# Kernel optimization log

Hardware: AMD Instinct MI355X
Metric: run time of the kernel (lower is better)

The kernel has to match this reference:

```python
import jax, jax.numpy as jnp
import numpy as np

D_K = 64  # per-head key dim, used for 1/sqrt(d_k) scaling


def setup_inputs() -> dict:
    key = jax.random.key(0)
    ks = jax.random.split(key, 9)
    B, S, D, H, DK, DV = 2, 4096, 512, 8, 64, 64
    s = 0.02
    return {
        "x": jax.random.normal(ks[0], (B, S, D), dtype=jnp.float32),
        "Wq": jax.random.normal(ks[1], (H, D, DK), dtype=jnp.float32) * s,
        "bq": jax.random.normal(ks[2], (H, DK), dtype=jnp.float32) * s,
        "Wk": jax.random.normal(ks[3], (H, D, DK), dtype=jnp.float32) * s,
        "bk": jax.random.normal(ks[4], (H, DK), dtype=jnp.float32) * s,
        "Wv": jax.random.normal(ks[5], (H, D, DV), dtype=jnp.float32) * s,
        "bv": jax.random.normal(ks[6], (H, DV), dtype=jnp.float32) * s,
        "Wo": jax.random.normal(ks[7], (H * DV, D), dtype=jnp.float32) * s,
        "bo": jax.random.normal(ks[8], (D,), dtype=jnp.float32) * s,
    }


def reference(x, Wq, bq, Wk, bk, Wv, bv, Wo, bo):
    # Per-head projections, vectorized over heads: [B,H,S,dk/dv]
    q = jnp.einsum("bsd,hdk->bhsk", x, Wq) + bq[None, :, None, :]
    k = jnp.einsum("bsd,hdk->bhsk", x, Wk) + bk[None, :, None, :]
    v = jnp.einsum("bsd,hdv->bhsv", x, Wv) + bv[None, :, None, :]
    # Scaled dot-product attention (no mask; dropout inactive at eval)
    scores = jnp.einsum("bhsk,bhtk->bhst", q, k) / jnp.sqrt(jnp.float32(D_K))
    attn = jax.nn.softmax(scores, axis=-1)
    o = jnp.einsum("bhst,bhtv->bhsv", attn, v)
    # Concat heads along feature dim: [B,S,H*dv]
    B, H, S, DV = o.shape
    concat = jnp.transpose(o, (0, 2, 1, 3)).reshape(B, S, H * DV)
    return concat @ Wo + bo
```

## Files before the change

kernel.cpp:

```cpp
#include <hip/hip_runtime.h>
#include <hip/hip_bf16.h>

typedef __attribute__((ext_vector_type(8))) short bf16x8;
typedef __attribute__((ext_vector_type(4))) float f32x4;
typedef __attribute__((ext_vector_type(16))) float f32x16;
typedef __attribute__((ext_vector_type(4))) unsigned short u16x4;
typedef __attribute__((ext_vector_type(4))) unsigned int u32x4;

#define NB 2
#define NS 4096
#define ND 512
#define NH 8

__device__ __forceinline__ unsigned short f2bf(float f) {
  unsigned int u = __float_as_uint(f);
  u += 0x7fffu + ((u >> 16) & 1u);
  return (unsigned short)(u >> 16);
}

__device__ __forceinline__ float bf2f(unsigned short h) {
  return __uint_as_float(((unsigned)h) << 16);
}

__device__ __forceinline__ float exp2_hw(float x) {
  float r;
  asm("v_exp_f32 %0, %1" : "=v"(r) : "v"(x));
  return r;
}

__device__ __forceinline__ unsigned cvtpk(float lo, float hi) {
  unsigned r;
  asm("v_cvt_pk_bf16_f32 %0, %1, %2" : "=v"(r) : "v"(lo), "v"(hi));
  return r;
}

__device__ __forceinline__ void swap32(unsigned& a, unsigned& b) {
  asm("v_permlane32_swap_b32 %0, %1" : "+v"(a), "+v"(b));
}

__device__ __forceinline__ bf16x8 mkfrag(unsigned w0, unsigned w1,
                                         unsigned w2, unsigned w3) {
  u32x4 u = {w0, w1, w2, w3};
  return __builtin_bit_cast(bf16x8, u);
}

__device__ __forceinline__ void gload_lds16(const unsigned short* g,
                                            unsigned short* l) {
  __builtin_amdgcn_global_load_lds(
      (const __attribute__((address_space(1))) unsigned int*)g,
      (__attribute__((address_space(3))) unsigned int*)l, 16, 0, 0);
}

__global__ void pack_kernel(const float* __restrict__ x,
                            const float* __restrict__ Wq,
                            const float* __restrict__ Wk,
                            const float* __restrict__ Wv,
                            const float* __restrict__ Wo,
                            unsigned short* __restrict__ x_bf,
                            unsigned short* __restrict__ w3,
                            unsigned short* __restrict__ wo_t)
{
  int idx = blockIdx.x * 256 + threadIdx.x;
  const int NX4 = NB * NS * ND / 4;
  const int NW = 512 * 512;
  if (idx < NX4) {
    const float4 f = ((const float4*)x)[idx];
    u16x4 o;
    o[0] = f2bf(f.x); o[1] = f2bf(f.y); o[2] = f2bf(f.z); o[3] = f2bf(f.w);
    ((u16x4*)x_bf)[idx] = o;
  } else if (idx < NX4 + 3 * NW) {
    int j = idx - NX4;
    int p = j / NW;
    int r = j - p * NW;
    int n = r >> 9, d = r & 511;
    int h = n >> 6, o = n & 63;
    const float* W = (p == 0) ? Wq : (p == 1) ? Wk : Wv;
    w3[j] = f2bf(W[(h * 512 + d) * 64 + o]);
  } else if (idx < NX4 + 4 * NW) {
    int j = idx - NX4 - 3 * NW;
    int n = j >> 9, kk = j & 511;
    wo_t[j] = f2bf(Wo[kk * 512 + n]);
  }
}

template <int MODE>
__global__ void gemm_bt(const unsigned short* __restrict__ A,
                        const unsigned short* __restrict__ Bm,
                        const float* __restrict__ b0,
                        const float* __restrict__ b1,
                        const float* __restrict__ b2,
                        unsigned short* __restrict__ qo,
                        unsigned short* __restrict__ ko,
                        unsigned short* __restrict__ vo,
                        float* __restrict__ fo) {
  __shared__ unsigned short Al[128 * 32];
  __shared__ unsigned short Bl[128 * 32];
  const int t = threadIdx.x;
  const int m0 = blockIdx.x * 128;
  const int n0 = blockIdx.y * 128;
  const int lane = t & 63;
  const int w = t >> 6;
  const int wm = w >> 1, wn = w & 1;
  const int c = lane & 15, g = lane >> 4;

  f32x4 acc[4][4];
#pragma unroll
  for (int i = 0; i < 4; ++i)
#pragma unroll
    for (int j = 0; j < 4; ++j) acc[i][j] = (f32x4){0.f, 0.f, 0.f, 0.f};

  const int srow = t >> 1, sseg = (t & 1) * 16;
  const unsigned short* Ap = A + (size_t)(m0 + srow) * 512 + sseg;
  const unsigned short* Bp = Bm + (size_t)(n0 + srow) * 512 + sseg;
  unsigned short* Alp = &Al[srow * 32 + sseg];
  unsigned short* Blp = &Bl[srow * 32 + sseg];

  for (int k0 = 0; k0 < 512; k0 += 32) {
    bf16x8 ra0 = *(const bf16x8*)(Ap + k0);
    bf16x8 ra1 = *(const bf16x8*)(Ap + k0 + 8);
    bf16x8 rb0 = *(const bf16x8*)(Bp + k0);
    bf16x8 rb1 = *(const bf16x8*)(Bp + k0 + 8);
    __syncthreads();
    *(bf16x8*)(Alp) = ra0;
    *(bf16x8*)(Alp + 8) = ra1;
    *(bf16x8*)(Blp) = rb0;
    *(bf16x8*)(Blp + 8) = rb1;
    __syncthreads();
    bf16x8 af[4], bfr[4];
#pragma unroll
    for (int mf = 0; mf < 4; ++mf)
      af[mf] = *(const bf16x8*)&Al[(wm * 64 + mf * 16 + c) * 32 + g * 8];
#pragma unroll
    for (int nf = 0; nf < 4; ++nf)
      bfr[nf] = *(const bf16x8*)&Bl[(wn * 64 + nf * 16 + c) * 32 + g * 8];
#pragma unroll
    for (int mf = 0; mf < 4; ++mf)
#pragma unroll
      for (int nf = 0; nf < 4; ++nf)
        acc[mf][nf] = __builtin_amdgcn_mfma_f32_16x16x32_bf16(
            af[mf], bfr[nf], acc[mf][nf], 0, 0, 0);
  }

  if (MODE == 0) {
    const int proj = n0 >> 9;
    const float* bias = proj == 0 ? b0 : (proj == 1 ? b1 : b2);
    unsigned short* dst01 = proj == 0 ? qo : ko;
    const float scale = proj == 0 ? 0.18033688011112042f : 1.0f;
#pragma unroll
    for (int nf = 0; nf < 4; ++nf) {
      const int col5 = (n0 + wn * 64 + nf * 16 + c) & 511;
      const int h = col5 >> 6, o = col5 & 63;
      const float bb = bias[col5];
#pragma unroll
      for (int mf = 0; mf < 4; ++mf) {
#pragma unroll
        for (int r = 0; r < 4; ++r) {
          const int m = m0 + wm * 64 + mf * 16 + g * 4 + r;
          const int b = m >> 12, s = m & 4095;
          const unsigned short hb = f2bf((acc[mf][nf][r] + bb) * scale);
          if (proj < 2)
            dst01[((size_t)((b * NH + h) * NS + s)) * 64 + o] = hb;
          else
            vo[((size_t)((b * NH + h) * 64 + o)) * NS + s] = hb;
        }
      }
    }
  } else {
#pragma unroll
    for (int nf = 0; nf < 4; ++nf) {
      const int col = n0 + wn * 64 + nf * 16 + c;
      const float bb = b0[col];
#pragma unroll
      for (int mf = 0; mf < 4; ++mf) {
#pragma unroll
        for (int r = 0; r < 4; ++r) {
          const int m = m0 + wm * 64 + mf * 16 + g * 4 + r;
          fo[(size_t)m * 512 + col] = acc[mf][nf][r] + bb;
        }
      }
    }
  }
}

__device__ __forceinline__ void softmax_qset_fm(f32x16& pA, f32x16& pB,
                                                float& l_, bf16x8* pb) {
#pragma unroll
  for (int r = 0; r < 16; ++r) {
    pA[r] = exp2_hw(pA[r]);
    pB[r] = exp2_hw(pB[r]);
  }
  float s[8];
#pragma unroll
  for (int r = 0; r < 8; ++r)
    s[r] = (pA[r] + pA[r + 8]) + (pB[r] + pB[r + 8]);
  float rs = ((s[0] + s[1]) + (s[2] + s[3])) + ((s[4] + s[5]) + (s[6] + s[7]));
  rs += __shfl_xor(rs, 32, 64);
  l_ += rs;
  unsigned g0[8], g1[8];
#pragma unroll
  for (int gg = 0; gg < 8; ++gg) {
    g0[gg] = cvtpk(pA[2 * gg], pA[2 * gg + 1]);
    g1[gg] = cvtpk(pB[2 * gg], pB[2 * gg + 1]);
  }
  unsigned a1, b1, c1, d1;
  a1 = g0[0]; b1 = g0[2]; swap32(a1, b1);
  c1 = g0[1]; d1 = g0[3]; swap32(c1, d1);
  pb[0] = mkfrag(a1, c1, b1, d1);
  a1 = g0[4]; b1 = g0[6]; swap32(a1, b1);
  c1 = g0[5]; d1 = g0[7]; swap32(c1, d1);
  pb[1] = mkfrag(a1, c1, b1, d1);
  a1 = g1[0]; b1 = g1[2]; swap32(a1, b1);
  c1 = g1[1]; d1 = g1[3]; swap32(c1, d1);
  pb[2] = mkfrag(a1, c1, b1, d1);
  a1 = g1[4]; b1 = g1[6]; swap32(a1, b1);
  c1 = g1[5]; d1 = g1[7]; swap32(c1, d1);
  pb[3] = mkfrag(a1, c1, b1, d1);
}

template <int SPLITS>
__global__ __launch_bounds__(256, 1) void attn_kernel(
    const unsigned short* __restrict__ q,
    const unsigned short* __restrict__ k,
    const unsigned short* __restrict__ vt,
    unsigned short* __restrict__ cc,
    unsigned short* __restrict__ op,
    float* __restrict__ ml)
{
  union SMemU {
    struct { unsigned short Kl[3][4096]; unsigned short Vl[3][4096]; } kv;
    unsigned short Ol[4][32][68];
  };
  __shared__ SMemU sm;
  const int t = threadIdx.x;
  const int w = t >> 6, lane = t & 63;
  const int col = lane & 31, hi = lane >> 5;
  const int bh = blockIdx.y & 15;
  const int sp = blockIdx.y >> 4;
  const int b = bh >> 3, h = bh & 7;
  const int q0 = blockIdx.x * 256 + w * 64;
  const int kbase = sp * (NS / SPLITS);

  const unsigned short* qh = q + (size_t)bh * NS * 64;
  const unsigned short* kh = k + (size_t)bh * NS * 64;
  const unsigned short* vh = vt + (size_t)bh * 64 * NS;

  bf16x8 qf[2][4];
#pragma unroll
  for (int qs = 0; qs < 2; ++qs)
#pragma unroll
    for (int c = 0; c < 4; ++c)
      qf[qs][c] = *(const bf16x8*)&qh[(size_t)(q0 + qs * 32 + col) * 64 +
                                      c * 16 + hi * 8];

  const int rl = lane >> 3, chn = lane & 7;
  const int lk = rl * 64 + ((chn ^ (rl & 7)) << 3);
  const int lv = rl * NS + ((chn ^ (rl & 7)) << 3);

  auto ISSUE = [&](int tile, int bi) {
    const unsigned short* gk = kh + (size_t)(kbase + tile * 64 + w * 16) * 64;
    const unsigned short* gv = vh + (size_t)(w * 16) * NS + kbase + tile * 64;
    gload_lds16(gk + lk, &sm.kv.Kl[bi][w * 1024]);
    gload_lds16(gk + lk + 512, &sm.kv.Kl[bi][w * 1024 + 512]);
    gload_lds16(gv + lv, &sm.kv.Vl[bi][w * 1024]);
    gload_lds16(gv + lv + 8 * NS, &sm.kv.Vl[bi][w * 1024 + 512]);
  };

  f32x16 ot[4];
#pragma unroll
  for (int i = 0; i < 4; ++i)
#pragma unroll
    for (int r = 0; r < 16; ++r) ot[i][r] = 0.f;
  float l_[2] = {0.f, 0.f};

  const int NT = NS / (64 * SPLITS);

  ISSUE(0, 0);
  if (NT > 1) ISSUE(1, 1);

  int cur = 0;
  for (int it = 0; it < NT; ++it) {
    if (it + 1 < NT)
      asm volatile("s_waitcnt vmcnt(4)" ::: "memory");
    else
      asm volatile("s_waitcnt vmcnt(0)" ::: "memory");
    __builtin_amdgcn_s_barrier();
    __builtin_amdgcn_sched_barrier(0);
    if (it + 2 < NT) {
      int b2 = cur + 2;
      if (b2 >= 3) b2 -= 3;
      ISSUE(it + 2, b2);
    }

    bf16x8 kfr[2][4];
#pragma unroll
    for (int c = 0; c < 4; ++c) {
      const int cidx = (((2 * c + hi) ^ (col & 7)) << 3);
      kfr[0][c] = *(const bf16x8*)&sm.kv.Kl[cur][col * 64 + cidx];
      kfr[1][c] = *(const bf16x8*)&sm.kv.Kl[cur][(col + 32) * 64 + cidx];
    }

    f32x16 p0, p1;
#pragma unroll
    for (int r = 0; r < 16; ++r) { p0[r] = 0.f; p1[r] = 0.f; }
    __builtin_amdgcn_s_setprio(1);
#pragma unroll
    for (int c = 0; c < 4; ++c) {
      p0 = __builtin_amdgcn_mfma_f32_32x32x16_bf16(kfr[0][c], qf[0][c], p0, 0, 0, 0);
      p1 = __builtin_amdgcn_mfma_f32_32x32x16_bf16(kfr[1][c], qf[0][c], p1, 0, 0, 0);
    }
    __builtin_amdgcn_s_setprio(0);

    bf16x8 pb0[4];
    softmax_qset_fm(p0, p1, l_[0], pb0);

    f32x16 p2, p3;
#pragma unroll
    for (int r = 0; r < 16; ++r) { p2[r] = 0.f; p3[r] = 0.f; }
    __builtin_amdgcn_s_setprio(1);
#pragma unroll
    for (int c = 0; c < 4; ++c) {
      p2 = __builtin_amdgcn_mfma_f32_32x32x16_bf16(kfr[0][c], qf[1][c], p2, 0, 0, 0);
      p3 = __builtin_amdgcn_mfma_f32_32x32x16_bf16(kfr[1][c], qf[1][c], p3, 0, 0, 0);
    }
    __builtin_amdgcn_s_setprio(0);

    bf16x8 vfr[2][4];
#pragma unroll
    for (int ks = 0; ks < 4; ++ks) {
      const int cidx = (((2 * ks + hi) ^ (col & 7)) << 3);
      vfr[0][ks] = *(const bf16x8*)&sm.kv.Vl[cur][col * 64 + cidx];
      vfr[1][ks] = *(const bf16x8*)&sm.kv.Vl[cur][(col + 32) * 64 + cidx];
    }
    __builtin_amdgcn_s_setprio(1);
#pragma unroll
    for (int ks = 0; ks < 4; ++ks) {
      ot[0] = __builtin_amdgcn_mfma_f32_32x32x16_bf16(vfr[0][ks], pb0[ks], ot[0], 0, 0, 0);
      ot[1] = __builtin_amdgcn_mfma_f32_32x32x16_bf16(vfr[1][ks], pb0[ks], ot[1], 0, 0, 0);
    }
    __builtin_amdgcn_s_setprio(0);

    bf16x8 pb1[4];
    softmax_qset_fm(p2, p3, l_[1], pb1);
    __builtin_amdgcn_s_setprio(1);
#pragma unroll
    for (int ks = 0; ks < 4; ++ks) {
      ot[2] = __builtin_amdgcn_mfma_f32_32x32x16_bf16(vfr[0][ks], pb1[ks], ot[2], 0, 0, 0);
      ot[3] = __builtin_amdgcn_mfma_f32_32x32x16_bf16(vfr[1][ks], pb1[ks], ot[3], 0, 0, 0);
    }
    __builtin_amdgcn_s_setprio(0);

    cur = (cur + 1 == 3) ? 0 : cur + 1;
  }

  __syncthreads();

#pragma unroll
  for (int qs = 0; qs < 2; ++qs) {
    const float inv = (SPLITS == 1) ? (1.0f / l_[qs]) : 1.0f;
#pragma unroll
    for (int r = 0; r < 16; ++r) {
      const int dvb = (r & 3) + 8 * (r >> 2) + 4 * hi;
      sm.Ol[w][col][dvb] = f2bf(ot[qs * 2][r] * inv);
      sm.Ol[w][col][dvb + 32] = f2bf(ot[qs * 2 + 1][r] * inv);
    }
    if (SPLITS > 1 && hi == 0)
      ml[(size_t)(sp * 16 + bh) * NS + q0 + qs * 32 + col] = l_[qs];
    asm volatile("s_waitcnt lgkmcnt(0)" ::: "memory");
    const int row = lane >> 1;
#pragma unroll
    for (int p = 0; p < 4; ++p) {
      const int chunk = (lane & 1) + 2 * p;
      bf16x8 vv = *(const bf16x8*)&sm.Ol[w][row][chunk * 8];
      if (SPLITS == 1)
        *(bf16x8*)&cc[((size_t)(b * NS + q0 + qs * 32 + row)) * 512 + h * 64 +
                      chunk * 8] = vv;
      else
        *(bf16x8*)&op[((size_t)(sp * 16 + bh) * NS + q0 + qs * 32 + row) * 64 +
                      chunk * 8] = vv;
    }
    asm volatile("s_waitcnt lgkmcnt(0)" ::: "memory");
  }
}

template <int SPLITS>
__global__ void combine_kernel(const unsigned short* __restrict__ op,
                               const float* __restrict__ ml,
                               unsigned short* __restrict__ cc) {
  const int id = blockIdx.x * 256 + threadIdx.x;
  const int chunk = id & 7;
  const int qq = (id >> 3) & 4095;
  const int bh = id >> 15;
  const int b = bh >> 3, h = bh & 7;
  float lsum = 0.f;
#pragma unroll
  for (int sp = 0; sp < SPLITS; ++sp)
    lsum += ml[(size_t)(sp * 16 + bh) * NS + qq];
  const float invl = 1.0f / lsum;
  float acc[8];
#pragma unroll
  for (int j = 0; j < 8; ++j) acc[j] = 0.f;
#pragma unroll
  for (int sp = 0; sp < SPLITS; ++sp) {
    const bf16x8 o =
        *(const bf16x8*)&op[((size_t)(sp * 16 + bh) * NS + qq) * 64 + chunk * 8];
#pragma unroll
    for (int j = 0; j < 8; ++j) acc[j] += bf2f((unsigned short)o[j]);
  }
  bf16x8 out;
#pragma unroll
  for (int j = 0; j < 8; ++j) out[j] = (short)f2bf(acc[j] * invl);
  *(bf16x8*)&cc[((size_t)(b * NS + qq)) * 512 + h * 64 + chunk * 8] = out;
}

extern "C" void kernel_launch(void* const* d_in, const int* in_sizes, int n_in,
                              void* d_out, int out_size, void* d_ws, size_t ws_size,
                              hipStream_t stream) {
  const float* x  = (const float*)d_in[0];
  const float* Wq = (const float*)d_in[1];
  const float* bq = (const float*)d_in[2];
  const float* Wk = (const float*)d_in[3];
  const float* bk = (const float*)d_in[4];
  const float* Wv = (const float*)d_in[5];
  const float* bv = (const float*)d_in[6];
  const float* Wo = (const float*)d_in[7];
  const float* bo = (const float*)d_in[8];

  unsigned char* ws = (unsigned char*)d_ws;
  unsigned short* x_bf = (unsigned short*)(ws);
  unsigned short* w3   = (unsigned short*)(ws + 8388608);
  unsigned short* wo_t = (unsigned short*)(ws + 9961472);
  unsigned short* qb   = (unsigned short*)(ws + 10485760);
  unsigned short* kb   = (unsigned short*)(ws + 18874368);
  unsigned short* vb   = (unsigned short*)(ws + 27262976);
  unsigned short* op   = (unsigned short*)(ws + 35651584);
  unsigned short* cc   = x_bf;

  const size_t need2 = 35651584ull + 2ull * 8388608 + 2ull * 16 * 4096 * 4;

  pack_kernel<<<8192, 256, 0, stream>>>(x, Wq, Wk, Wv, Wo, x_bf, w3, wo_t);
  gemm_bt<0><<<dim3(64, 12), 256, 0, stream>>>(x_bf, w3, bq, bk, bv, qb, kb, vb,
                                               nullptr);
  if (ws_size >= need2) {
    float* mlp = (float*)(ws + 35651584 + 2ull * 8388608);
    attn_kernel<2><<<dim3(16, 32), 256, 0, stream>>>(qb, kb, vb, nullptr, op,
                                                     mlp);
    combine_kernel<2><<<2048, 256, 0, stream>>>(op, mlp, cc);
  } else {
    attn_kernel<1><<<dim3(16, 16), 256, 0, stream>>>(qb, kb, vb, cc, nullptr,
                                                     nullptr);
  }
  gemm_bt<1><<<dim3(64, 4), 256, 0, stream>>>(cc, wo_t, bo, nullptr, nullptr,
                                              nullptr, nullptr, nullptr,
                                              (float*)d_out);
}
```

Measured before the change: 163.2 us.

## Halve per-wave query tile and double-buffer KV to fit two blocks per CU

Each wave now handles 32 query rows instead of 64, so the grid doubles and register use drops. The KV LDS ring shrinks from triple to double buffering, and the launch bound allows two blocks per CU. The intent is to hide latency through occupancy rather than in-wave interleaving of two query sets. The cost is that each K/V tile loaded into LDS is reused by half as many queries, and only one tile is prefetched ahead, with a full vmcnt(0) wait each iteration.

```diff
diff --git a/kernel.cpp b/kernel.cpp
--- a/kernel.cpp
+++ b/kernel.cpp
@@ -182,43 +182,8 @@
   }
 }
 
-__device__ __forceinline__ void softmax_qset_fm(f32x16& pA, f32x16& pB,
-                                                float& l_, bf16x8* pb) {
-#pragma unroll
-  for (int r = 0; r < 16; ++r) {
-    pA[r] = exp2_hw(pA[r]);
-    pB[r] = exp2_hw(pB[r]);
-  }
-  float s[8];
-#pragma unroll
-  for (int r = 0; r < 8; ++r)
-    s[r] = (pA[r] + pA[r + 8]) + (pB[r] + pB[r + 8]);
-  float rs = ((s[0] + s[1]) + (s[2] + s[3])) + ((s[4] + s[5]) + (s[6] + s[7]));
-  rs += __shfl_xor(rs, 32, 64);
-  l_ += rs;
-  unsigned g0[8], g1[8];
-#pragma unroll
-  for (int gg = 0; gg < 8; ++gg) {
-    g0[gg] = cvtpk(pA[2 * gg], pA[2 * gg + 1]);
-    g1[gg] = cvtpk(pB[2 * gg], pB[2 * gg + 1]);
-  }
-  unsigned a1, b1, c1, d1;
-  a1 = g0[0]; b1 = g0[2]; swap32(a1, b1);
-  c1 = g0[1]; d1 = g0[3]; swap32(c1, d1);
-  pb[0] = mkfrag(a1, c1, b1, d1);
-  a1 = g0[4]; b1 = g0[6]; swap32(a1, b1);
-  c1 = g0[5]; d1 = g0[7]; swap32(c1, d1);
-  pb[1] = mkfrag(a1, c1, b1, d1);
-  a1 = g1[0]; b1 = g1[2]; swap32(a1, b1);
-  c1 = g1[1]; d1 = g1[3]; swap32(c1, d1);
-  pb[2] = mkfrag(a1, c1, b1, d1);
-  a1 = g1[4]; b1 = g1[6]; swap32(a1, b1);
-  c1 = g1[5]; d1 = g1[7]; swap32(c1, d1);
-  pb[3] = mkfrag(a1, c1, b1, d1);
-}
-
 template <int SPLITS>
-__global__ __launch_bounds__(256, 1) void attn_kernel(
+__global__ __launch_bounds__(256, 2) void attn_kernel(
     const unsigned short* __restrict__ q,
     const unsigned short* __restrict__ k,
     const unsigned short* __restrict__ vt,
@@ -227,7 +192,7 @@
     float* __restrict__ ml)
 {
   union SMemU {
-    struct { unsigned short Kl[3][4096]; unsigned short Vl[3][4096]; } kv;
+    struct { unsigned short Kl[2][4096]; unsigned short Vl[2][4096]; } kv;
     unsigned short Ol[4][32][68];
   };
   __shared__ SMemU sm;
@@ -237,20 +202,17 @@
   const int bh = blockIdx.y & 15;
   const int sp = blockIdx.y >> 4;
   const int b = bh >> 3, h = bh & 7;
-  const int q0 = blockIdx.x * 256 + w * 64;
+  const int q0 = blockIdx.x * 128 + w * 32;
   const int kbase = sp * (NS / SPLITS);
 
   const unsigned short* qh = q + (size_t)bh * NS * 64;
   const unsigned short* kh = k + (size_t)bh * NS * 64;
   const unsigned short* vh = vt + (size_t)bh * 64 * NS;
 
-  bf16x8 qf[2][4];
-#pragma unroll
-  for (int qs = 0; qs < 2; ++qs)
-#pragma unroll
-    for (int c = 0; c < 4; ++c)
-      qf[qs][c] = *(const bf16x8*)&qh[(size_t)(q0 + qs * 32 + col) * 64 +
-                                      c * 16 + hi * 8];
+  bf16x8 qf[4];
+#pragma unroll
+  for (int c = 0; c < 4; ++c)
+    qf[c] = *(const bf16x8*)&qh[(size_t)(q0 + col) * 64 + c * 16 + hi * 8];
 
   const int rl = lane >> 3, chn = lane & 7;
   const int lk = rl * 64 + ((chn ^ (rl & 7)) << 3);
@@ -265,31 +227,21 @@
     gload_lds16(gv + lv + 8 * NS, &sm.kv.Vl[bi][w * 1024 + 512]);
   };
 
-  f32x16 ot[4];
-#pragma unroll
-  for (int i = 0; i < 4; ++i)
-#pragma unroll
-    for (int r = 0; r < 16; ++r) ot[i][r] = 0.f;
-  float l_[2] = {0.f, 0.f};
+  f32x16 ot0, ot1;
+#pragma unroll
+  for (int r = 0; r < 16; ++r) { ot0[r] = 0.f; ot1[r] = 0.f; }
+  float l_ = 0.f;
 
   const int NT = NS / (64 * SPLITS);
 
   ISSUE(0, 0);
-  if (NT > 1) ISSUE(1, 1);
-
-  int cur = 0;
+
   for (int it = 0; it < NT; ++it) {
-    if (it + 1 < NT)
-      asm volatile("s_waitcnt vmcnt(4)" ::: "memory");
-    else
-      asm volatile("s_waitcnt vmcnt(0)" ::: "memory");
+    const int cur = it & 1;
+    asm volatile("s_waitcnt vmcnt(0)" ::: "memory");
     __builtin_amdgcn_s_barrier();
     __builtin_amdgcn_sched_barrier(0);
-    if (it + 2 < NT) {
-      int b2 = cur + 2;
-      if (b2 >= 3) b2 -= 3;
-      ISSUE(it + 2, b2);
-    }
+    if (it + 1 < NT) ISSUE(it + 1, cur ^ 1);
 
     bf16x8 kfr[2][4];
 #pragma unroll
@@ -298,29 +250,14 @@
       kfr[0][c] = *(const bf16x8*)&sm.kv.Kl[cur][col * 64 + cidx];
       kfr[1][c] = *(const bf16x8*)&sm.kv.Kl[cur][(col + 32) * 64 + cidx];
     }
-
     f32x16 p0, p1;
 #pragma unroll
     for (int r = 0; r < 16; ++r) { p0[r] = 0.f; p1[r] = 0.f; }
     __builtin_amdgcn_s_setprio(1);
 #pragma unroll
     for (int c = 0; c < 4; ++c) {
-      p0 = __builtin_amdgcn_mfma_f32_32x32x16_bf16(kfr[0][c], qf[0][c], p0, 0, 0, 0);
-      p1 = __builtin_amdgcn_mfma_f32_32x32x16_bf16(kfr[1][c], qf[0][c], p1, 0, 0, 0);
-    }
-    __builtin_amdgcn_s_setprio(0);
-
-    bf16x8 pb0[4];
-    softmax_qset_fm(p0, p1, l_[0], pb0);
-
-    f32x16 p2, p3;
-#pragma unroll
-    for (int r = 0; r < 16; ++r) { p2[r] = 0.f; p3[r] = 0.f; }
-    __builtin_amdgcn_s_setprio(1);
-#pragma unroll
-    for (int c = 0; c < 4; ++c) {
-      p2 = __builtin_amdgcn_mfma_f32_32x32x16_bf16(kfr[0][c], qf[1][c], p2, 0, 0, 0);
-      p3 = __builtin_amdgcn_mfma_f32_32x32x16_bf16(kfr[1][c], qf[1][c], p3, 0, 0, 0);
+      p0 = __builtin_amdgcn_mfma_f32_32x32x16_bf16(kfr[0][c], qf[c], p0, 0, 0, 0);
+      p1 = __builtin_amdgcn_mfma_f32_32x32x16_bf16(kfr[1][c], qf[c], p1, 0, 0, 0);
     }
     __builtin_amdgcn_s_setprio(0);
 
@@ -331,54 +268,77 @@
       vfr[0][ks] = *(const bf16x8*)&sm.kv.Vl[cur][col * 64 + cidx];
       vfr[1][ks] = *(const bf16x8*)&sm.kv.Vl[cur][(col + 32) * 64 + cidx];
     }
+
+#pragma unroll
+    for (int r = 0; r < 16; ++r) {
+      p0[r] = exp2_hw(p0[r]);
+      p1[r] = exp2_hw(p1[r]);
+    }
+    {
+      float s[8];
+#pragma unroll
+      for (int r = 0; r < 8; ++r)
+        s[r] = (p0[r] + p0[r + 8]) + (p1[r] + p1[r + 8]);
+      float rs =
+          ((s[0] + s[1]) + (s[2] + s[3])) + ((s[4] + s[5]) + (s[6] + s[7]));
+      rs += __shfl_xor(rs, 32, 64);
+      l_ += rs;
+    }
+    bf16x8 pb[4];
+    {
+      unsigned g0[8], g1[8];
+#pragma unroll
+      for (int gg = 0; gg < 8; ++gg) {
+        g0[gg] = cvtpk(p0[2 * gg], p0[2 * gg + 1]);
+        g1[gg] = cvtpk(p1[2 * gg], p1[2 * gg + 1]);
+      }
+      unsigned a1, b1, c1, d1;
+      a1 = g0[0]; b1 = g0[2]; swap32(a1, b1);
+      c1 = g0[1]; d1 = g0[3]; swap32(c1, d1);
+      pb[0] = mkfrag(a1, c1, b1, d1);
+      a1 = g0[4]; b1 = g0[6]; swap32(a1, b1);
+      c1 = g0[5]; d1 = g0[7]; swap32(c1, d1);
+      pb[1] = mkfrag(a1, c1, b1, d1);
+      a1 = g1[0]; b1 = g1[2]; swap32(a1, b1);
+      c1 = g1[1]; d1 = g1[3]; swap32(c1, d1);
+      pb[2] = mkfrag(a1, c1, b1, d1);
+      a1 = g1[4]; b1 = g1[6]; swap32(a1, b1);
+      c1 = g1[5]; d1 = g1[7]; swap32(c1, d1);
+      pb[3] = mkfrag(a1, c1, b1, d1);
+    }
+
     __builtin_amdgcn_s_setprio(1);
 #pragma unroll
     for (int ks = 0; ks < 4; ++ks) {
-      ot[0] = __builtin_amdgcn_mfma_f32_32x32x16_bf16(vfr[0][ks], pb0[ks], ot[0], 0, 0, 0);
-      ot[1] = __builtin_amdgcn_mfma_f32_32x32x16_bf16(vfr[1][ks], pb0[ks], ot[1], 0, 0, 0);
+      ot0 = __builtin_amdgcn_mfma_f32_32x32x16_bf16(vfr[0][ks], pb[ks], ot0, 0, 0, 0);
+      ot1 = __builtin_amdgcn_mfma_f32_32x32x16_bf16(vfr[1][ks], pb[ks], ot1, 0, 0, 0);
     }
     __builtin_amdgcn_s_setprio(0);
-
-    bf16x8 pb1[4];
-    softmax_qset_fm(p2, p3, l_[1], pb1);
-    __builtin_amdgcn_s_setprio(1);
-#pragma unroll
-    for (int ks = 0; ks < 4; ++ks) {
-      ot[2] = __builtin_amdgcn_mfma_f32_32x32x16_bf16(vfr[0][ks], pb1[ks], ot[2], 0, 0, 0);
-      ot[3] = __builtin_amdgcn_mfma_f32_32x32x16_bf16(vfr[1][ks], pb1[ks], ot[3], 0, 0, 0);
-    }
-    __builtin_amdgcn_s_setprio(0);
-
-    cur = (cur + 1 == 3) ? 0 : cur + 1;
   }
 
   __syncthreads();
 
-#pragma unroll
-  for (int qs = 0; qs < 2; ++qs) {
-    const float inv = (SPLITS == 1) ? (1.0f / l_[qs]) : 1.0f;
-#pragma unroll
-    for (int r = 0; r < 16; ++r) {
-      const int dvb = (r & 3) + 8 * (r >> 2) + 4 * hi;
-      sm.Ol[w][col][dvb] = f2bf(ot[qs * 2][r] * inv);
-      sm.Ol[w][col][dvb + 32] = f2bf(ot[qs * 2 + 1][r] * inv);
-    }
-    if (SPLITS > 1 && hi == 0)
-      ml[(size_t)(sp * 16 + bh) * NS + q0 + qs * 32 + col] = l_[qs];
-    asm volatile("s_waitcnt lgkmcnt(0)" ::: "memory");
-    const int row = lane >> 1;
-#pragma unroll
-    for (int p = 0; p < 4; ++p) {
-      const int chunk = (lane & 1) + 2 * p;
-      bf16x8 vv = *(const bf16x8*)&sm.Ol[w][row][chunk * 8];
-      if (SPLITS == 1)
-        *(bf16x8*)&cc[((size_t)(b * NS + q0 + qs * 32 + row)) * 512 + h * 64 +
-                      chunk * 8] = vv;
-      else
-        *(bf16x8*)&op[((size_t)(sp * 16 + bh) * NS + q0 + qs * 32 + row) * 64 +
-                      chunk * 8] = vv;
-    }
-    asm volatile("s_waitcnt lgkmcnt(0)" ::: "memory");
+  const float inv = (SPLITS == 1) ? (1.0f / l_) : 1.0f;
+#pragma unroll
+  for (int r = 0; r < 16; ++r) {
+    const int dvb = (r & 3) + 8 * (r >> 2) + 4 * hi;
+    sm.Ol[w][col][dvb] = f2bf(ot0[r] * inv);
+    sm.Ol[w][col][dvb + 32] = f2bf(ot1[r] * inv);
+  }
+  if (SPLITS > 1 && hi == 0)
+    ml[(size_t)(sp * 16 + bh) * NS + q0 + col] = l_;
+  asm volatile("s_waitcnt lgkmcnt(0)" ::: "memory");
+  const int row = lane >> 1;
+#pragma unroll
+  for (int p = 0; p < 4; ++p) {
+    const int chunk = (lane & 1) + 2 * p;
+    bf16x8 vv = *(const bf16x8*)&sm.Ol[w][row][chunk * 8];
+    if (SPLITS == 1)
+      *(bf16x8*)&cc[((size_t)(b * NS + q0 + row)) * 512 + h * 64 + chunk * 8] =
+          vv;
+    else
+      *(bf16x8*)&op[((size_t)(sp * 16 + bh) * NS + q0 + row) * 64 + chunk * 8] =
+          vv;
   }
 }
 
@@ -442,11 +402,11 @@
                                                nullptr);
   if (ws_size >= need2) {
     float* mlp = (float*)(ws + 35651584 + 2ull * 8388608);
-    attn_kernel<2><<<dim3(16, 32), 256, 0, stream>>>(qb, kb, vb, nullptr, op,
+    attn_kernel<2><<<dim3(32, 32), 256, 0, stream>>>(qb, kb, vb, nullptr, op,
                                                      mlp);
     combine_kernel<2><<<2048, 256, 0, stream>>>(op, mlp, cc);
   } else {
-    attn_kernel<1><<<dim3(16, 16), 256, 0, stream>>>(qb, kb, vb, cc, nullptr,
+    attn_kernel<1><<<dim3(32, 16), 256, 0, stream>>>(qb, kb, vb, cc, nullptr,
                                                      nullptr);
   }
   gemm_bt<1><<<dim3(64, 4), 256, 0, stream>>>(cc, wo_t, bo, nullptr, nullptr,
```

Measured after the change: 145.9 us. 1.12x faster.
